# Kernel optimization log

Hardware: AMD Instinct MI355X
Metric: run time of the kernel (lower is better)

The kernel has to match this reference:

```python
import jax, jax.numpy as jnp
import numpy as np

C = 128                      # channels per irrep
LS = [0, 0, 1, 1, 2, 2]      # active irreps (0e,0o,1e,1o,2e,2o), sorted order
D = C * sum(2 * l + 1 for l in LS)  # 2304
N = 100000                   # nodes


def setup_inputs() -> dict:
    key = jax.random.key(0)
    ks = jax.random.split(key, 7)
    inp = {"x": jax.random.normal(ks[0], (N, D), dtype=jnp.float32)}
    scale = 1.0 / np.sqrt(C)
    for name, k in zip(["W0p", "W0m", "W1p", "W1m", "W2p", "W2m"], ks[1:]):
        inp[name] = jax.random.normal(k, (C, C), dtype=jnp.float32) * scale
    return inp


def reference(x, W0p, W0m, W1p, W1m, W2p, W2m):
    # Split flat features into per-(l,parity) blocks [N, C, 2l+1],
    # mix channels per irrep (movedim + Linear in torch == einsum here),
    # merge back and add residual.
    Ws = [W0p, W0m, W1p, W1m, W2p, W2m]
    idx = 0
    parts = []
    for l, W in zip(LS, Ws):
        d = C * (2 * l + 1)
        blk = x[:, idx:idx + d].reshape(-1, C, 2 * l + 1)  # [N, C, m]
        idx += d
        y = jnp.einsum('ncm,dc->ndm', blk, W)              # channel mix per m
        parts.append(y.reshape(-1, d))
    return x + jnp.concatenate(parts, axis=-1)
```

## Files before the change

### kernel.cpp

```cpp
#include <hip/hip_runtime.h>
#include <hip/hip_bf16.h>

typedef float f32x4 __attribute__((ext_vector_type(4)));
typedef short s16x8 __attribute__((ext_vector_type(8)));

#define SMEM_BYTES 24576

__device__ __forceinline__ unsigned short f32_to_bf16(float f){
    union { float f; unsigned u; } v; v.f = f;
    unsigned r = v.u + 0x7fffu + ((v.u >> 16) & 1u);
    return (unsigned short)(r >> 16);
}
__device__ __forceinline__ unsigned pack2(float a, float b){
    float2 t; t.x = a; t.y = b;
    __hip_bfloat162 h = __float22bfloat162_rn(t);
    union { __hip_bfloat162 h; unsigned u; } c; c.h = h;
    return c.u;
}

__global__ __launch_bounds__(256)
void wconv_kernel(const float* __restrict__ W0p, const float* __restrict__ W0m,
                  const float* __restrict__ W1p, const float* __restrict__ W1m,
                  const float* __restrict__ W2p, const float* __restrict__ W2m,
                  unsigned short* __restrict__ wbf)
{
    const int idx = blockIdx.x * 256 + threadIdx.x;
    const int w  = idx >> 14;
    const int rc = idx & 16383;
    const float* Wp;
    switch (w) {
        case 0: Wp = W0p; break;  case 1: Wp = W0m; break;
        case 2: Wp = W1p; break;  case 3: Wp = W1m; break;
        case 4: Wp = W2p; break;  default: Wp = W2m; break;
    }
    const float v = Wp[rc] + (((rc >> 7) == (rc & 127)) ? 1.0f : 0.0f);
    wbf[idx] = f32_to_bf16(v);
}

template<int ML, int NT>
__device__ __forceinline__
void lx_body(const float* __restrict__ src0, const unsigned short* __restrict__ wb,
             float* __restrict__ dst0, int tile, char* smem)
{
    constexpr int BLK   = 128 * ML;
    constexpr int RROWS = NT * ML;
    constexpr int RTC   = (RROWS + 15) / 16;
    constexpr int H     = (RTC + 1) / 2;
    constexpr int LDSS  = 136;
    constexpr int QPT   = NT * 32 / 256;
    constexpr int ITER  = NT * BLK / 1024;

    unsigned short* lin  = (unsigned short*)smem;
    float*          lout = (float*)smem;

    const size_t nbase = (size_t)tile * NT;
    const int tid = threadIdx.x;
    const int wv  = tid >> 6, ln = tid & 63;
    const int l16 = ln & 15,  lhi = ln >> 4;

    const float* src = src0 + nbase * 2304;
    #pragma unroll
    for (int i = 0; i < QPT; ++i) {
        const int q  = i * 256 + tid;
        const int nl = q >> 5;
        const int c4 = (q & 31) * 4;
        const float* p = src + (size_t)nl * 2304 + c4 * ML;
        float v[4 * ML];
        #pragma unroll
        for (int j = 0; j < ML; ++j) {
            const float4 t = *reinterpret_cast<const float4*>(p + j * 4);
            v[j*4+0] = t.x; v[j*4+1] = t.y; v[j*4+2] = t.z; v[j*4+3] = t.w;
        }
        #pragma unroll
        for (int mm = 0; mm < ML; ++mm) {
            uint2 pk;
            pk.x = pack2(v[mm], v[mm + ML]);
            pk.y = pack2(v[mm + 2*ML], v[mm + 3*ML]);
            *reinterpret_cast<uint2*>(&lin[(nl * ML + mm) * LDSS + c4]) = pk;
        }
    }
    __syncthreads();

    const int th = wv >> 1, ch = wv & 1;
    const int t0 = th * H;

    f32x4 acc[H][4];
    #pragma unroll
    for (int rt = 0; rt < H; ++rt)
        #pragma unroll
        for (int tf = 0; tf < 4; ++tf) acc[rt][tf] = (f32x4){0.f,0.f,0.f,0.f};

    #pragma unroll
    for (int s = 0; s < 4; ++s) {
        const int k0 = s * 32 + lhi * 8;
        s16x8 bf[4];
        #pragma unroll
        for (int tf = 0; tf < 4; ++tf)
            bf[tf] = *reinterpret_cast<const s16x8*>(wb + (ch * 64 + tf * 16 + l16) * 128 + k0);
        #pragma unroll
        for (int rt = 0; rt < H; ++rt) {
            if (t0 + rt < RTC) {
                const s16x8 af = *reinterpret_cast<const s16x8*>(
                    &lin[((t0 + rt) * 16 + l16) * LDSS + k0]);
                #pragma unroll
                for (int tf = 0; tf < 4; ++tf)
                    acc[rt][tf] = __builtin_amdgcn_mfma_f32_16x16x32_bf16(af, bf[tf], acc[rt][tf], 0, 0, 0);
            }
        }
    }
    __syncthreads();

    #pragma unroll
    for (int rt = 0; rt < H; ++rt) {
        if (t0 + rt < RTC) {
            #pragma unroll
            for (int tf = 0; tf < 4; ++tf) {
                const int col = ch * 64 + tf * 16 + l16;
                #pragma unroll
                for (int j = 0; j < 4; ++j) {
                    const int row = (t0 + rt) * 16 + lhi * 4 + j;
                    if (row < RROWS) {
                        const int nl = row / ML;
                        const int mm = row - nl * ML;
                        lout[nl * BLK + col * ML + mm] = acc[rt][tf][j];
                    }
                }
            }
        }
    }
    __syncthreads();

    float* dst = dst0 + nbase * 2304;
    #pragma unroll
    for (int i = 0; i < ITER; ++i) {
        const int f  = (i * 256 + tid) * 4;
        const int nl = f / BLK;
        const int rr = f - nl * BLK;
        *reinterpret_cast<float4*>(dst + (size_t)nl * 2304 + rr) =
            *reinterpret_cast<const float4*>(&lout[f]);
    }
}

__device__ __forceinline__
void l0_body(const float* __restrict__ x, const unsigned short* __restrict__ wbf,
             float* __restrict__ out, int tile, char* smem)
{
    constexpr int LDSS = 264;
    unsigned short* lin = (unsigned short*)smem;

    const size_t nbase = (size_t)tile * 32;
    const int tid = threadIdx.x;
    const int wv  = tid >> 6, ln = tid & 63;
    const int l16 = ln & 15,  lhi = ln >> 4;

    const float* src = x + nbase * 2304;
    #pragma unroll
    for (int i = 0; i < 8; ++i) {
        const int f  = i * 1024 + tid * 4;
        const int nl = f >> 8, c = f & 255;
        const float4 v = *reinterpret_cast<const float4*>(src + (size_t)nl * 2304 + c);
        uint2 p; p.x = pack2(v.x, v.y); p.y = pack2(v.z, v.w);
        *reinterpret_cast<uint2*>(&lin[nl * LDSS + c]) = p;
    }
    __syncthreads();

    const int b     = wv >> 1;
    const int dbase = (wv & 1) * 64;
    const unsigned short* wb = wbf + b * 16384;

    f32x4 acc[2][4];
    #pragma unroll
    for (int nt = 0; nt < 2; ++nt)
        #pragma unroll
        for (int dt = 0; dt < 4; ++dt) acc[nt][dt] = (f32x4){0.f,0.f,0.f,0.f};

    #pragma unroll
    for (int s = 0; s < 4; ++s) {
        const int k0 = s * 32 + lhi * 8;
        s16x8 af[4];
        #pragma unroll
        for (int dt = 0; dt < 4; ++dt)
            af[dt] = *reinterpret_cast<const s16x8*>(wb + (dbase + dt * 16 + l16) * 128 + k0);
        #pragma unroll
        for (int nt = 0; nt < 2; ++nt) {
            const s16x8 bfv = *reinterpret_cast<const s16x8*>(
                &lin[(nt * 16 + l16) * LDSS + b * 128 + k0]);
            #pragma unroll
            for (int dt = 0; dt < 4; ++dt)
                acc[nt][dt] = __builtin_amdgcn_mfma_f32_16x16x32_bf16(af[dt], bfv, acc[nt][dt], 0, 0, 0);
        }
    }

    #pragma unroll
    for (int nt = 0; nt < 2; ++nt) {
        float* dst = out + (nbase + nt * 16 + l16) * 2304 + b * 128 + dbase + lhi * 4;
        #pragma unroll
        for (int dt = 0; dt < 4; ++dt) {
            float4 v; v.x = acc[nt][dt][0]; v.y = acc[nt][dt][1];
                      v.z = acc[nt][dt][2]; v.w = acc[nt][dt][3];
            *reinterpret_cast<float4*>(dst + dt * 16) = v;
        }
    }
}

__global__ __launch_bounds__(256)
void fused_kernel(const float* __restrict__ x, const unsigned short* __restrict__ wbf,
                  float* __restrict__ out)
{
    __shared__ __attribute__((aligned(16))) char smem[SMEM_BYTES];
    const int bucket = blockIdx.x / 13;
    const int r      = blockIdx.x - bucket * 13;

    if (r < 8) {
        const int idx    = bucket * 8 + r;
        const int parity = idx & 1;
        const int tile   = idx >> 1;
        const int off    = parity ? 1664 : 1024;
        lx_body<5, 8>(x + off, wbf + (size_t)(4 + parity) * 16384, out + off, tile, smem);
    } else if (r < 12) {
        const int idx    = bucket * 4 + (r - 8);
        const int parity = idx & 1;
        const int tile   = idx >> 1;
        const int off    = parity ? 640 : 256;
        lx_body<3, 16>(x + off, wbf + (size_t)(2 + parity) * 16384, out + off, tile, smem);
    } else {
        l0_body(x, wbf, out, bucket, smem);
    }
}

extern "C" void kernel_launch(void* const* d_in, const int* in_sizes, int n_in,
                              void* d_out, int out_size, void* d_ws, size_t ws_size,
                              hipStream_t stream) {
    const float* x   = (const float*)d_in[0];
    const float* W0p = (const float*)d_in[1];
    const float* W0m = (const float*)d_in[2];
    const float* W1p = (const float*)d_in[3];
    const float* W1m = (const float*)d_in[4];
    const float* W2p = (const float*)d_in[5];
    const float* W2m = (const float*)d_in[6];
    float* out = (float*)d_out;
    unsigned short* wbf = (unsigned short*)d_ws;

    wconv_kernel<<<384, 256, 0, stream>>>(W0p, W0m, W1p, W1m, W2p, W2m, wbf);
    fused_kernel<<<40625, 256, 0, stream>>>(x, wbf, out);
}
```

Before: 478.5 us.

## Split fused kernel into persistent per-irrep kernels with register prefetch pipelining

Replaces the single bucketed kernel with three persistent grid-stride kernels (l=2, l=1, l=0). Each block keeps its weight fragments in registers and prefetches the next tile's global loads into registers while the current tile is being computed and stored. Tile sizes shrink (l=1 from 16 to 8 nodes, l=0 from 32 to 16), and occupancy is hinted at 4 blocks per CU. In exchange, the work runs as three separate launches instead of one mixed launch, and register pressure rises from the prefetch buffers.

```diff
diff --git a/kernel.cpp b/kernel.cpp
--- a/kernel.cpp
+++ b/kernel.cpp
@@ -3,8 +3,6 @@
 
 typedef float f32x4 __attribute__((ext_vector_type(4)));
 typedef short s16x8 __attribute__((ext_vector_type(8)));
-
-#define SMEM_BYTES 24576
 
 __device__ __forceinline__ unsigned short f32_to_bf16(float f){
     union { float f; unsigned u; } v; v.f = f;
@@ -16,6 +14,12 @@
     __hip_bfloat162 h = __float22bfloat162_rn(t);
     union { __hip_bfloat162 h; unsigned u; } c; c.h = h;
     return c.u;
+}
+
+__device__ __forceinline__ void wg_barrier(){
+    asm volatile("s_waitcnt lgkmcnt(0)" ::: "memory");
+    __builtin_amdgcn_s_barrier();
+    __builtin_amdgcn_sched_barrier(0);
 }
 
 __global__ __launch_bounds__(256)
@@ -38,9 +42,9 @@
 }
 
 template<int ML, int NT>
-__device__ __forceinline__
-void lx_body(const float* __restrict__ src0, const unsigned short* __restrict__ wb,
-             float* __restrict__ dst0, int tile, char* smem)
+__global__ __launch_bounds__(256, 4)
+void lx_pipe(const float* __restrict__ x, const unsigned short* __restrict__ wbf,
+             float* __restrict__ out, int yoff0, int yoff1, int w0, int ntiles)
 {
     constexpr int BLK   = 128 * ML;
     constexpr int RROWS = NT * ML;
@@ -49,182 +53,211 @@
     constexpr int LDSS  = 136;
     constexpr int QPT   = NT * 32 / 256;
     constexpr int ITER  = NT * BLK / 1024;
-
+    constexpr int IN_B  = RTC * 16 * LDSS * 2;
+    constexpr int OUT_B = NT * BLK * 4;
+    constexpr int SMEM  = OUT_B > IN_B ? OUT_B : IN_B;
+    __shared__ __attribute__((aligned(16))) char smem[SMEM];
     unsigned short* lin  = (unsigned short*)smem;
     float*          lout = (float*)smem;
 
-    const size_t nbase = (size_t)tile * NT;
+    const int parity = blockIdx.y;
+    const int yoff   = parity ? yoff1 : yoff0;
+    const unsigned short* wb = wbf + (size_t)(w0 + parity) * 16384;
+
     const int tid = threadIdx.x;
     const int wv  = tid >> 6, ln = tid & 63;
     const int l16 = ln & 15,  lhi = ln >> 4;
-
-    const float* src = src0 + nbase * 2304;
+    const int th  = wv >> 1,  ch = wv & 1;
+    const int t0  = th * H;
+
+    s16x8 bfr[4][4];
     #pragma unroll
-    for (int i = 0; i < QPT; ++i) {
-        const int q  = i * 256 + tid;
-        const int nl = q >> 5;
-        const int c4 = (q & 31) * 4;
-        const float* p = src + (size_t)nl * 2304 + c4 * ML;
-        float v[4 * ML];
-        #pragma unroll
-        for (int j = 0; j < ML; ++j) {
-            const float4 t = *reinterpret_cast<const float4*>(p + j * 4);
-            v[j*4+0] = t.x; v[j*4+1] = t.y; v[j*4+2] = t.z; v[j*4+3] = t.w;
-        }
-        #pragma unroll
-        for (int mm = 0; mm < ML; ++mm) {
-            uint2 pk;
-            pk.x = pack2(v[mm], v[mm + ML]);
-            pk.y = pack2(v[mm + 2*ML], v[mm + 3*ML]);
-            *reinterpret_cast<uint2*>(&lin[(nl * ML + mm) * LDSS + c4]) = pk;
-        }
-    }
-    __syncthreads();
-
-    const int th = wv >> 1, ch = wv & 1;
-    const int t0 = th * H;
-
-    f32x4 acc[H][4];
-    #pragma unroll
-    for (int rt = 0; rt < H; ++rt)
-        #pragma unroll
-        for (int tf = 0; tf < 4; ++tf) acc[rt][tf] = (f32x4){0.f,0.f,0.f,0.f};
-
-    #pragma unroll
-    for (int s = 0; s < 4; ++s) {
-        const int k0 = s * 32 + lhi * 8;
-        s16x8 bf[4];
+    for (int s = 0; s < 4; ++s)
         #pragma unroll
         for (int tf = 0; tf < 4; ++tf)
-            bf[tf] = *reinterpret_cast<const s16x8*>(wb + (ch * 64 + tf * 16 + l16) * 128 + k0);
+            bfr[s][tf] = *reinterpret_cast<const s16x8*>(
+                wb + (ch * 64 + tf * 16 + l16) * 128 + s * 32 + lhi * 8);
+
+    float4 buf[QPT][ML];
+    auto issue = [&](int t) {
+        const float* src = x + yoff + (size_t)t * NT * 2304;
+        #pragma unroll
+        for (int i = 0; i < QPT; ++i) {
+            const int q  = i * 256 + tid;
+            const int nl = q >> 5;
+            const int c4 = (q & 31) * 4;
+            const float* p = src + (size_t)nl * 2304 + c4 * ML;
+            #pragma unroll
+            for (int j = 0; j < ML; ++j)
+                buf[i][j] = *reinterpret_cast<const float4*>(p + j * 4);
+        }
+    };
+
+    issue(blockIdx.x);
+
+    for (int tile = blockIdx.x; tile < ntiles; ) {
+        const int next = tile + (int)gridDim.x;
+
+        wg_barrier();
+
+        #pragma unroll
+        for (int i = 0; i < QPT; ++i) {
+            const int q  = i * 256 + tid;
+            const int nl = q >> 5;
+            const int c4 = (q & 31) * 4;
+            float v[4 * ML];
+            #pragma unroll
+            for (int j = 0; j < ML; ++j) {
+                v[j*4+0] = buf[i][j].x; v[j*4+1] = buf[i][j].y;
+                v[j*4+2] = buf[i][j].z; v[j*4+3] = buf[i][j].w;
+            }
+            #pragma unroll
+            for (int mm = 0; mm < ML; ++mm) {
+                uint2 pk;
+                pk.x = pack2(v[mm],        v[mm +   ML]);
+                pk.y = pack2(v[mm + 2*ML], v[mm + 3*ML]);
+                *reinterpret_cast<uint2*>(&lin[(nl * ML + mm) * LDSS + c4]) = pk;
+            }
+        }
+
+        if (next < ntiles) issue(next);
+
+        wg_barrier();
+
+        f32x4 acc[H][4];
+        #pragma unroll
+        for (int rt = 0; rt < H; ++rt)
+            #pragma unroll
+            for (int tf = 0; tf < 4; ++tf) acc[rt][tf] = (f32x4){0.f,0.f,0.f,0.f};
+
+        #pragma unroll
+        for (int s = 0; s < 4; ++s) {
+            const int k0 = s * 32 + lhi * 8;
+            #pragma unroll
+            for (int rt = 0; rt < H; ++rt) {
+                if (t0 + rt < RTC) {
+                    const s16x8 af = *reinterpret_cast<const s16x8*>(
+                        &lin[((t0 + rt) * 16 + l16) * LDSS + k0]);
+                    #pragma unroll
+                    for (int tf = 0; tf < 4; ++tf)
+                        acc[rt][tf] = __builtin_amdgcn_mfma_f32_16x16x32_bf16(
+                            af, bfr[s][tf], acc[rt][tf], 0, 0, 0);
+                }
+            }
+        }
+
+        wg_barrier();
+
         #pragma unroll
         for (int rt = 0; rt < H; ++rt) {
             if (t0 + rt < RTC) {
-                const s16x8 af = *reinterpret_cast<const s16x8*>(
-                    &lin[((t0 + rt) * 16 + l16) * LDSS + k0]);
                 #pragma unroll
-                for (int tf = 0; tf < 4; ++tf)
-                    acc[rt][tf] = __builtin_amdgcn_mfma_f32_16x16x32_bf16(af, bf[tf], acc[rt][tf], 0, 0, 0);
-            }
-        }
-    }
-    __syncthreads();
-
-    #pragma unroll
-    for (int rt = 0; rt < H; ++rt) {
-        if (t0 + rt < RTC) {
-            #pragma unroll
-            for (int tf = 0; tf < 4; ++tf) {
-                const int col = ch * 64 + tf * 16 + l16;
-                #pragma unroll
-                for (int j = 0; j < 4; ++j) {
-                    const int row = (t0 + rt) * 16 + lhi * 4 + j;
-                    if (row < RROWS) {
-                        const int nl = row / ML;
-                        const int mm = row - nl * ML;
-                        lout[nl * BLK + col * ML + mm] = acc[rt][tf][j];
+                for (int tf = 0; tf < 4; ++tf) {
+                    const int col = ch * 64 + tf * 16 + l16;
+                    #pragma unroll
+                    for (int j = 0; j < 4; ++j) {
+                        const int row = (t0 + rt) * 16 + lhi * 4 + j;
+                        if (row < RROWS) {
+                            const int nl = row / ML;
+                            const int mm = row - nl * ML;
+                            lout[nl * BLK + col * ML + mm] = acc[rt][tf][j];
+                        }
                     }
                 }
             }
         }
+
+        wg_barrier();
+
+        {
+            float* dst = out + yoff + (size_t)tile * NT * 2304;
+            #pragma unroll
+            for (int i = 0; i < ITER; ++i) {
+                const int f  = (i * 256 + tid) * 4;
+                const int nl = f / BLK;
+                const int rr = f - nl * BLK;
+                *reinterpret_cast<float4*>(dst + (size_t)nl * 2304 + rr) =
+                    *reinterpret_cast<const float4*>(&lout[f]);
+            }
+        }
+        tile = next;
     }
-    __syncthreads();
-
-    float* dst = dst0 + nbase * 2304;
-    #pragma unroll
-    for (int i = 0; i < ITER; ++i) {
-        const int f  = (i * 256 + tid) * 4;
-        const int nl = f / BLK;
-        const int rr = f - nl * BLK;
-        *reinterpret_cast<float4*>(dst + (size_t)nl * 2304 + rr) =
-            *reinterpret_cast<const float4*>(&lout[f]);
-    }
-}
-
-__device__ __forceinline__
-void l0_body(const float* __restrict__ x, const unsigned short* __restrict__ wbf,
-             float* __restrict__ out, int tile, char* smem)
+}
+
+__global__ __launch_bounds__(256, 4)
+void l0_pipe(const float* __restrict__ x, const unsigned short* __restrict__ wbf,
+             float* __restrict__ out, int ntiles)
 {
     constexpr int LDSS = 264;
-    unsigned short* lin = (unsigned short*)smem;
-
-    const size_t nbase = (size_t)tile * 32;
+    __shared__ __attribute__((aligned(16))) unsigned short lin[16 * LDSS];
+
     const int tid = threadIdx.x;
     const int wv  = tid >> 6, ln = tid & 63;
     const int l16 = ln & 15,  lhi = ln >> 4;
-
-    const float* src = x + nbase * 2304;
-    #pragma unroll
-    for (int i = 0; i < 8; ++i) {
-        const int f  = i * 1024 + tid * 4;
-        const int nl = f >> 8, c = f & 255;
-        const float4 v = *reinterpret_cast<const float4*>(src + (size_t)nl * 2304 + c);
-        uint2 p; p.x = pack2(v.x, v.y); p.y = pack2(v.z, v.w);
-        *reinterpret_cast<uint2*>(&lin[nl * LDSS + c]) = p;
-    }
-    __syncthreads();
-
     const int b     = wv >> 1;
     const int dbase = (wv & 1) * 64;
     const unsigned short* wb = wbf + b * 16384;
 
-    f32x4 acc[2][4];
+    s16x8 afr[4][4];
     #pragma unroll
-    for (int nt = 0; nt < 2; ++nt)
-        #pragma unroll
-        for (int dt = 0; dt < 4; ++dt) acc[nt][dt] = (f32x4){0.f,0.f,0.f,0.f};
-
-    #pragma unroll
-    for (int s = 0; s < 4; ++s) {
-        const int k0 = s * 32 + lhi * 8;
-        s16x8 af[4];
+    for (int s = 0; s < 4; ++s)
         #pragma unroll
         for (int dt = 0; dt < 4; ++dt)
-            af[dt] = *reinterpret_cast<const s16x8*>(wb + (dbase + dt * 16 + l16) * 128 + k0);
-        #pragma unroll
-        for (int nt = 0; nt < 2; ++nt) {
+            afr[s][dt] = *reinterpret_cast<const s16x8*>(
+                wb + (dbase + dt * 16 + l16) * 128 + s * 32 + lhi * 8);
+
+    float4 buf[4];
+    auto issue = [&](int t) {
+        const float* src = x + (size_t)t * 16 * 2304;
+        #pragma unroll
+        for (int i = 0; i < 4; ++i) {
+            const int f  = i * 1024 + tid * 4;
+            const int nl = f >> 8, c = f & 255;
+            buf[i] = *reinterpret_cast<const float4*>(src + (size_t)nl * 2304 + c);
+        }
+    };
+
+    issue(blockIdx.x);
+
+    for (int tile = blockIdx.x; tile < ntiles; ) {
+        const int next = tile + (int)gridDim.x;
+
+        wg_barrier();
+
+        #pragma unroll
+        for (int i = 0; i < 4; ++i) {
+            const int f  = i * 1024 + tid * 4;
+            const int nl = f >> 8, c = f & 255;
+            uint2 p; p.x = pack2(buf[i].x, buf[i].y); p.y = pack2(buf[i].z, buf[i].w);
+            *reinterpret_cast<uint2*>(&lin[nl * LDSS + c]) = p;
+        }
+
+        if (next < ntiles) issue(next);
+
+        wg_barrier();
+
+        f32x4 acc[4];
+        #pragma unroll
+        for (int dt = 0; dt < 4; ++dt) acc[dt] = (f32x4){0.f,0.f,0.f,0.f};
+
+        #pragma unroll
+        for (int s = 0; s < 4; ++s) {
             const s16x8 bfv = *reinterpret_cast<const s16x8*>(
-                &lin[(nt * 16 + l16) * LDSS + b * 128 + k0]);
+                &lin[l16 * LDSS + b * 128 + s * 32 + lhi * 8]);
             #pragma unroll
             for (int dt = 0; dt < 4; ++dt)
-                acc[nt][dt] = __builtin_amdgcn_mfma_f32_16x16x32_bf16(af[dt], bfv, acc[nt][dt], 0, 0, 0);
-        }
-    }
-
-    #pragma unroll
-    for (int nt = 0; nt < 2; ++nt) {
-        float* dst = out + (nbase + nt * 16 + l16) * 2304 + b * 128 + dbase + lhi * 4;
+                acc[dt] = __builtin_amdgcn_mfma_f32_16x16x32_bf16(
+                    afr[s][dt], bfv, acc[dt], 0, 0, 0);
+        }
+
+        float* dst = out + ((size_t)tile * 16 + l16) * 2304 + b * 128 + dbase + lhi * 4;
         #pragma unroll
         for (int dt = 0; dt < 4; ++dt) {
-            float4 v; v.x = acc[nt][dt][0]; v.y = acc[nt][dt][1];
-                      v.z = acc[nt][dt][2]; v.w = acc[nt][dt][3];
-            *reinterpret_cast<float4*>(dst + dt * 16) = v;
-        }
-    }
-}
-
-__global__ __launch_bounds__(256)
-void fused_kernel(const float* __restrict__ x, const unsigned short* __restrict__ wbf,
-                  float* __restrict__ out)
-{
-    __shared__ __attribute__((aligned(16))) char smem[SMEM_BYTES];
-    const int bucket = blockIdx.x / 13;
-    const int r      = blockIdx.x - bucket * 13;
-
-    if (r < 8) {
-        const int idx    = bucket * 8 + r;
-        const int parity = idx & 1;
-        const int tile   = idx >> 1;
-        const int off    = parity ? 1664 : 1024;
-        lx_body<5, 8>(x + off, wbf + (size_t)(4 + parity) * 16384, out + off, tile, smem);
-    } else if (r < 12) {
-        const int idx    = bucket * 4 + (r - 8);
-        const int parity = idx & 1;
-        const int tile   = idx >> 1;
-        const int off    = parity ? 640 : 256;
-        lx_body<3, 16>(x + off, wbf + (size_t)(2 + parity) * 16384, out + off, tile, smem);
-    } else {
-        l0_body(x, wbf, out, bucket, smem);
+            float4 vv; vv.x = acc[dt][0]; vv.y = acc[dt][1];
+                       vv.z = acc[dt][2]; vv.w = acc[dt][3];
+            *reinterpret_cast<float4*>(dst + dt * 16) = vv;
+        }
+        tile = next;
     }
 }
 
@@ -241,6 +274,11 @@
     float* out = (float*)d_out;
     unsigned short* wbf = (unsigned short*)d_ws;
 
+    const int N = in_sizes[0] / 2304;
+
     wconv_kernel<<<384, 256, 0, stream>>>(W0p, W0m, W1p, W1m, W2p, W2m, wbf);
-    fused_kernel<<<40625, 256, 0, stream>>>(x, wbf, out);
-}
+
+    lx_pipe<5, 8><<<dim3(2048, 2), 256, 0, stream>>>(x, wbf, out, 1024, 1664, 4, N / 8);
+    lx_pipe<3, 8><<<dim3(2048, 2), 256, 0, stream>>>(x, wbf, out, 256,  640,  2, N / 8);
+    l0_pipe      <<<2048,          256, 0, stream>>>(x, wbf, out, N / 16);
+}
```

After: 540.0 us. +12.9%, slower.
